# Performance work log

Measured on AMD Instinct MI355X. Metric: run time of the kernel, lower is better.

Reference implementation:

```python
import jax, jax.numpy as jnp
import numpy as np


def _hfreq_mask(c, scale):
    # zeros over the centered (shifted) low-frequency band, ones elsewhere
    m = np.ones((c,), dtype=np.complex64)
    m[c // 2 - c // scale: c // 2 + c // scale] = 0
    return jnp.asarray(m).reshape(1, 1, 1, c)


def setup_inputs() -> dict:
    key = jax.random.key(0)
    x = jax.random.normal(key, (32, 38, 38, 728), dtype=jnp.float32)
    return {"x": x, "scale": 4}


def reference(x, scale):
    c = x.shape[-1]
    norm = jnp.asarray(np.sqrt(c), dtype=jnp.complex64)
    X = jnp.fft.fft(x.astype(jnp.complex64), axis=-1) / norm
    X = jnp.fft.fftshift(X, axes=-1)
    X = X * _hfreq_mask(c, scale)
    X = jnp.fft.ifftshift(X, axes=-1)
    y = jnp.fft.ifft(X, axis=-1) * norm
    y = jnp.real(y).astype(jnp.float32)
    return jax.nn.relu(y)
```

## Files before the change

### kernel.cpp

```cpp
#include <hip/hip_runtime.h>
#include <hip/hip_bf16.h>

#define CC 728
#define PP 364
#define KP 384
#define KT 12
#define ROWS 32
#define NWG 1444

typedef __attribute__((ext_vector_type(8))) short bf16x8;
typedef __attribute__((ext_vector_type(8))) unsigned short ushort8;
typedef __attribute__((ext_vector_type(4))) float f32x4;

__device__ __forceinline__ unsigned int f2bf(float f) {
    unsigned int u = __float_as_uint(f);
    unsigned int r = u + 0x7fffu + ((u >> 16) & 1u);
    return r >> 16;
}

__device__ __forceinline__ float bf2f(unsigned short v) {
    unsigned int u = ((unsigned int)v) << 16;
    return __uint_as_float(u);
}

__global__ void build_bt(unsigned short* __restrict__ bt1,
                         unsigned short* __restrict__ bt2) {
    int idx = blockIdx.x * blockDim.x + threadIdx.x;
    if (idx >= 2 * KP * KP) return;
    int mat = idx / (KP * KP);
    int rem = idx % (KP * KP);
    int n = rem / KP, k = rem % KP;
    float v = 0.f;
    if (n < PP && k < PP) {
        int m = n - k - (mat == 0 ? 1 : 0);
        if (m < 0) m += PP;
        int d = 2 * m + 1;
        float t = (float)(3.14159265358979323846 * (double)d / (double)CC);
        float s = ((d >> 1) & 1) ? 1.f : -1.f;
        v = s * cosf(t) / ((float)CC * sinf(t));
    }
    (mat == 0 ? bt1 : bt2)[n * KP + k] = (unsigned short)f2bf(v);
}

__global__ __launch_bounds__(512, 4) void fused_gemm_relu(
        const float* __restrict__ x,
        const unsigned short* __restrict__ bt1,
        const unsigned short* __restrict__ bt2,
        float* __restrict__ out) {
    __shared__ unsigned short ldsE[ROWS * KP];
    __shared__ unsigned short ldsO[ROWS * KP];

    const int tid  = threadIdx.x;
    const int lane = tid & 63;
    const int wid  = tid >> 6;
    const int l15  = lane & 15, lhi = lane >> 4;

    const int bm = blockIdx.x * ROWS;

#pragma unroll
    for (int i = 0; i < 3; ++i) {
        int idx = i * 512 + tid;
        int row = idx / 48, p8 = idx % 48;
        int c0  = p8 * 16;
        ushort8 ve, vo;
#pragma unroll
        for (int j = 0; j < 8; ++j) { ve[j] = 0; vo[j] = 0; }
        const float4* src = (const float4*)(x + (size_t)(bm + row) * CC + c0);
#pragma unroll
        for (int j = 0; j < 4; ++j) {
            if (c0 + 4 * j < CC) {
                float4 f = src[j];
                ve[2 * j]     = (unsigned short)f2bf(f.x);
                vo[2 * j]     = (unsigned short)f2bf(f.y);
                ve[2 * j + 1] = (unsigned short)f2bf(f.z);
                vo[2 * j + 1] = (unsigned short)f2bf(f.w);
            }
        }
        int pw = p8 ^ (row & 7);
        *(ushort8*)&ldsE[row * KP + pw * 8] = ve;
        *(ushort8*)&ldsO[row * KP + pw * 8] = vo;
    }
    __syncthreads();

    f32x4 acc_e[2][3], acc_o[2][3];
#pragma unroll
    for (int i = 0; i < 2; ++i)
#pragma unroll
        for (int j = 0; j < 3; ++j)
#pragma unroll
            for (int rr = 0; rr < 4; ++rr) { acc_e[i][j][rr] = 0.f; acc_o[i][j][rr] = 0.f; }

    const unsigned short* b1p[3];
    const unsigned short* b2p[3];
#pragma unroll
    for (int nf = 0; nf < 3; ++nf) {
        size_t off = (size_t)(wid * 48 + nf * 16 + l15) * KP + lhi * 8;
        b1p[nf] = bt1 + off;
        b2p[nf] = bt2 + off;
    }

#pragma unroll
    for (int kt = 0; kt < KT; ++kt) {
        bf16x8 b1[3], b2[3];
#pragma unroll
        for (int nf = 0; nf < 3; ++nf) {
            b1[nf] = *(const bf16x8*)(b1p[nf] + kt * 32);
            b2[nf] = *(const bf16x8*)(b2p[nf] + kt * 32);
        }
        bf16x8 aE[2], aO[2];
#pragma unroll
        for (int mi = 0; mi < 2; ++mi) {
            int row = mi * 16 + l15;
            int c   = (kt * 4 + lhi) ^ (row & 7);
            aE[mi] = *(const bf16x8*)&ldsE[row * KP + c * 8];
            aO[mi] = *(const bf16x8*)&ldsO[row * KP + c * 8];
        }
#pragma unroll
        for (int mi = 0; mi < 2; ++mi)
#pragma unroll
            for (int nf = 0; nf < 3; ++nf) {
                acc_e[mi][nf] = __builtin_amdgcn_mfma_f32_16x16x32_bf16(
                    aO[mi], b1[nf], acc_e[mi][nf], 0, 0, 0);
                acc_o[mi][nf] = __builtin_amdgcn_mfma_f32_16x16x32_bf16(
                    aE[mi], b2[nf], acc_o[mi][nf], 0, 0, 0);
            }
    }

#pragma unroll
    for (int mi = 0; mi < 2; ++mi) {
#pragma unroll
        for (int nf = 0; nf < 3; ++nf) {
            int colp = wid * 48 + nf * 16 + l15;
            if (colp < PP) {
                int cch = colp >> 3;
#pragma unroll
                for (int rr = 0; rr < 4; ++rr) {
                    int lrow = mi * 16 + lhi * 4 + rr;
                    int cw   = cch ^ (lrow & 7);
                    float fe = bf2f(ldsE[lrow * KP + cw * 8 + (colp & 7)]);
                    float fo = bf2f(ldsO[lrow * KP + cw * 8 + (colp & 7)]);
                    float ye = 0.5f * fe + acc_e[mi][nf][rr];
                    float yo = 0.5f * fo + acc_o[mi][nf][rr];
                    float2 ov;
                    ov.x = ye > 0.f ? ye : 0.f;
                    ov.y = yo > 0.f ? yo : 0.f;
                    *(float2*)&out[(size_t)(bm + lrow) * CC + 2 * colp] = ov;
                }
            }
        }
    }
}

extern "C" void kernel_launch(void* const* d_in, const int* in_sizes, int n_in,
                              void* d_out, int out_size, void* d_ws, size_t ws_size,
                              hipStream_t stream) {
    const float* x = (const float*)d_in[0];
    float* out = (float*)d_out;

    unsigned short* bt1 = (unsigned short*)d_ws;
    unsigned short* bt2 = bt1 + KP * KP;

    build_bt<<<(2 * KP * KP + 255) / 256, 256, 0, stream>>>(bt1, bt2);
    fused_gemm_relu<<<NWG, 512, 0, stream>>>(x, bt1, bt2, out);
}
```

Measured before the change: 132.4 us.

## Stage B matrix tiles into double-buffered LDS via async global-to-LDS loads

```diff
diff --git a/kernel.cpp b/kernel.cpp
--- a/kernel.cpp
+++ b/kernel.cpp
@@ -23,6 +23,13 @@
     return __uint_as_float(u);
 }
 
+__device__ __forceinline__ void gload_lds16(const void* g, void* l) {
+    __builtin_amdgcn_global_load_lds(
+        (const __attribute__((address_space(1))) void*)g,
+        (__attribute__((address_space(3))) void*)l,
+        16, 0, 0);
+}
+
 __global__ void build_bt(unsigned short* __restrict__ bt1,
                          unsigned short* __restrict__ bt2) {
     int idx = blockIdx.x * blockDim.x + threadIdx.x;
@@ -42,21 +49,36 @@
     (mat == 0 ? bt1 : bt2)[n * KP + k] = (unsigned short)f2bf(v);
 }
 
-__global__ __launch_bounds__(512, 4) void fused_gemm_relu(
+__global__ __launch_bounds__(512, 2) void fused_gemm_relu(
         const float* __restrict__ x,
         const unsigned short* __restrict__ bt1,
         const unsigned short* __restrict__ bt2,
         float* __restrict__ out) {
-    __shared__ unsigned short ldsE[ROWS * KP];
-    __shared__ unsigned short ldsO[ROWS * KP];
+    __shared__ unsigned short ldsE[48 * 32 * 8];
+    __shared__ unsigned short ldsO[48 * 32 * 8];
+    __shared__ unsigned short ldsB1[2][1536 * 8];
+    __shared__ unsigned short ldsB2[2][1536 * 8];
 
     const int tid  = threadIdx.x;
     const int lane = tid & 63;
     const int wid  = tid >> 6;
     const int l15  = lane & 15, lhi = lane >> 4;
+    const int bm   = blockIdx.x * ROWS;
+    const int nb   = wid * 48;
 
-    const int bm = blockIdx.x * ROWS;
+    auto stageB = [&](int buf, int kt) {
+        int k0 = kt * 32;
+#pragma unroll
+        for (int i = 0; i < 3; ++i) {
+            int c  = i * 512 + tid;
+            int lc = c / 384, n = c % 384;
+            size_t so = (size_t)n * KP + k0 + lc * 8;
+            gload_lds16(bt1 + so, &ldsB1[buf][c * 8]);
+            gload_lds16(bt2 + so, &ldsB2[buf][c * 8]);
+        }
+    };
 
+    stageB(0, 0);
 #pragma unroll
     for (int i = 0; i < 3; ++i) {
         int idx = i * 512 + tid;
@@ -76,11 +98,12 @@
                 vo[2 * j + 1] = (unsigned short)f2bf(f.w);
             }
         }
-        int pw = p8 ^ (row & 7);
-        *(ushort8*)&ldsE[row * KP + pw * 8] = ve;
-        *(ushort8*)&ldsO[row * KP + pw * 8] = vo;
+        int rsw = row ^ ((p8 & 15) << 1);
+        *(ushort8*)&ldsE[(p8 * 32 + rsw) * 8] = ve;
+        *(ushort8*)&ldsO[(p8 * 32 + rsw) * 8] = vo;
     }
     __syncthreads();
+    stageB(1, 1);
 
     f32x4 acc_e[2][3], acc_o[2][3];
 #pragma unroll
@@ -90,31 +113,22 @@
 #pragma unroll
             for (int rr = 0; rr < 4; ++rr) { acc_e[i][j][rr] = 0.f; acc_o[i][j][rr] = 0.f; }
 
-    const unsigned short* b1p[3];
-    const unsigned short* b2p[3];
+    auto compute = [&](int buf, int kt) {
+        bf16x8 aE[2], aO[2], b1[3], b2[3];
+        const int kc = kt * 4 + lhi;
 #pragma unroll
-    for (int nf = 0; nf < 3; ++nf) {
-        size_t off = (size_t)(wid * 48 + nf * 16 + l15) * KP + lhi * 8;
-        b1p[nf] = bt1 + off;
-        b2p[nf] = bt2 + off;
-    }
-
-#pragma unroll
-    for (int kt = 0; kt < KT; ++kt) {
-        bf16x8 b1[3], b2[3];
+        for (int mi = 0; mi < 2; ++mi) {
+            int rsw = (mi * 16 + l15) ^ ((kc & 15) << 1);
+            aE[mi] = *(const bf16x8*)&ldsE[(kc * 32 + rsw) * 8];
+            aO[mi] = *(const bf16x8*)&ldsO[(kc * 32 + rsw) * 8];
+        }
 #pragma unroll
         for (int nf = 0; nf < 3; ++nf) {
-            b1[nf] = *(const bf16x8*)(b1p[nf] + kt * 32);
-            b2[nf] = *(const bf16x8*)(b2p[nf] + kt * 32);
+            int n = nb + nf * 16 + l15;
+            b1[nf] = *(const bf16x8*)&ldsB1[buf][(lhi * 384 + n) * 8];
+            b2[nf] = *(const bf16x8*)&ldsB2[buf][(lhi * 384 + n) * 8];
         }
-        bf16x8 aE[2], aO[2];
-#pragma unroll
-        for (int mi = 0; mi < 2; ++mi) {
-            int row = mi * 16 + l15;
-            int c   = (kt * 4 + lhi) ^ (row & 7);
-            aE[mi] = *(const bf16x8*)&ldsE[row * KP + c * 8];
-            aO[mi] = *(const bf16x8*)&ldsO[row * KP + c * 8];
-        }
+        __builtin_amdgcn_s_setprio(1);
 #pragma unroll
         for (int mi = 0; mi < 2; ++mi)
 #pragma unroll
@@ -124,27 +138,45 @@
                 acc_o[mi][nf] = __builtin_amdgcn_mfma_f32_16x16x32_bf16(
                     aE[mi], b2[nf], acc_o[mi][nf], 0, 0, 0);
             }
+        __builtin_amdgcn_s_setprio(0);
+    };
+
+    compute(0, 0);
+    __builtin_amdgcn_s_barrier();
+    __builtin_amdgcn_sched_barrier(0);
+    stageB(0, 2);
+
+#pragma unroll
+    for (int t = 1; t < KT; ++t) {
+        if (t + 1 < KT) asm volatile("s_waitcnt vmcnt(6)" ::: "memory");
+        else            asm volatile("s_waitcnt vmcnt(0)" ::: "memory");
+        __builtin_amdgcn_sched_barrier(0);
+        __builtin_amdgcn_s_barrier();
+        compute(t & 1, t);
+        __builtin_amdgcn_s_barrier();
+        __builtin_amdgcn_sched_barrier(0);
+        if (t + 2 < KT) stageB(t & 1, t + 2);
     }
 
 #pragma unroll
     for (int mi = 0; mi < 2; ++mi) {
 #pragma unroll
         for (int nf = 0; nf < 3; ++nf) {
-            int colp = wid * 48 + nf * 16 + l15;
+            int colp = nb + nf * 16 + l15;
             if (colp < PP) {
-                int cch = colp >> 3;
+                int kc = colp >> 3, el = colp & 7;
 #pragma unroll
                 for (int rr = 0; rr < 4; ++rr) {
-                    int lrow = mi * 16 + lhi * 4 + rr;
-                    int cw   = cch ^ (lrow & 7);
-                    float fe = bf2f(ldsE[lrow * KP + cw * 8 + (colp & 7)]);
-                    float fo = bf2f(ldsO[lrow * KP + cw * 8 + (colp & 7)]);
+                    int row = mi * 16 + lhi * 4 + rr;
+                    int rsw = row ^ ((kc & 15) << 1);
+                    float fe = bf2f(ldsE[(kc * 32 + rsw) * 8 + el]);
+                    float fo = bf2f(ldsO[(kc * 32 + rsw) * 8 + el]);
                     float ye = 0.5f * fe + acc_e[mi][nf][rr];
                     float yo = 0.5f * fo + acc_o[mi][nf][rr];
                     float2 ov;
                     ov.x = ye > 0.f ? ye : 0.f;
                     ov.y = yo > 0.f ? yo : 0.f;
-                    *(float2*)&out[(size_t)(bm + lrow) * CC + 2 * colp] = ov;
+                    *(float2*)&out[(size_t)(bm + row) * CC + 2 * colp] = ov;
                 }
             }
         }
```

Result: slower. 305.2 us (+130.6%).
